# Performance work log

Hardware: AMD Instinct MI355X
Metric: run time of the kernel (lower is better)

The kernel has to match this reference:

```python
import jax, jax.numpy as jnp
import numpy as np

B, S, I, H = 64, 512, 512, 512


def setup_inputs() -> dict:
    key = jax.random.key(0)
    ks = jax.random.split(key, 5)
    scale = 1.0 / np.sqrt(I + H)  # keep gates out of hard saturation
    return {
        "x": jax.random.normal(ks[0], (B, S, I), dtype=jnp.float32),
        "h": jax.random.normal(ks[1], (B, H), dtype=jnp.float32),
        "W_r": jax.random.normal(ks[2], (H, I + H), dtype=jnp.float32) * scale,
        "b_r": jnp.zeros((H,), dtype=jnp.float32),
        "W_z": jax.random.normal(ks[3], (H, I + H), dtype=jnp.float32) * scale,
        "b_z": jnp.zeros((H,), dtype=jnp.float32),
        "W_h": jax.random.normal(ks[4], (H, I + H), dtype=jnp.float32) * scale,
        "b_h": jnp.zeros((H,), dtype=jnp.float32),
    }


def reference(x, h, W_r, b_r, W_z, b_z, W_h, b_h):
    # Split each [H, I+H] weight into input part and hidden part (torch cat order: [x, h]).
    i = x.shape[-1]
    Wr_x, Wr_h = W_r[:, :i], W_r[:, i:]
    Wz_x, Wz_h = W_z[:, :i], W_z[:, i:]
    Wh_x, Wh_h = W_h[:, :i], W_h[:, i:]

    # Precompute the input contributions for all timesteps in one big GEMM each.
    xr = jnp.einsum("bsi,hi->bsh", x, Wr_x) + b_r  # [B,S,H]
    xz = jnp.einsum("bsi,hi->bsh", x, Wz_x) + b_z
    xh = jnp.einsum("bsi,hi->bsh", x, Wh_x) + b_h

    def step(h, inp):
        xr_t, xz_t, xh_t = inp  # each [B,H]
        r = jax.nn.sigmoid(xr_t + h @ Wr_h.T)
        z = jax.nn.sigmoid(xz_t + h @ Wz_h.T)
        h_tilde = jnp.tanh(xh_t + (r * h) @ Wh_h.T)
        h_new = (1.0 - z) * h + z * h_tilde
        return h_new, h_new

    # time-major for scan
    xs = (xr.transpose(1, 0, 2), xz.transpose(1, 0, 2), xh.transpose(1, 0, 2))
    h_last, ys = jax.lax.scan(step, h, xs)
    y = ys.transpose(1, 0, 2)  # [B,S,H]; dropout p=0 -> identity
    return y, h_last
```

## Files before the change

### kernel.cpp

```cpp
#include <hip/hip_runtime.h>

#define B_ 64
#define S_ 512
#define H_ 512

typedef unsigned short u16;
typedef unsigned int   u32;
typedef unsigned long long u64;

typedef __attribute__((ext_vector_type(8))) short    bf16x8;
typedef __attribute__((ext_vector_type(8))) _Float16 f16x8;
typedef __attribute__((ext_vector_type(4))) float    f32x4;
typedef __attribute__((ext_vector_type(2))) _Float16 h2_t;

#define PJ_GATE ((size_t)512 * 64 * 512)

__device__ inline u16 f2bf(float f) {
  u32 u = __builtin_bit_cast(u32, f);
  u32 r = (u + 0x7fffu + ((u >> 16) & 1u)) >> 16;
  return (u16)r;
}
__device__ inline u32 pkbf2(float a, float b) {
  return (u32)f2bf(a) | ((u32)f2bf(b) << 16);
}
__device__ inline u16 f2h(float a) {
  _Float16 x = (_Float16)a;
  return __builtin_bit_cast(u16, x);
}
__device__ inline u32 pk2h(float a, float b) {
  return (u32)f2h(a) | ((u32)f2h(b) << 16);
}
__device__ inline float sigmoidf_(float x) { return 1.f / (1.f + __expf(-x)); }
__device__ inline float tanhf_(float x) {
  float e = __expf(-2.f * fabsf(x));
  float t = (1.f - e) / (1.f + e);
  return copysignf(t, x);
}
__device__ inline void xstore64(u64* p, u64 v) {
  __hip_atomic_store(p, v, __ATOMIC_RELAXED, __HIP_MEMORY_SCOPE_AGENT);
}
__device__ inline u64 xload(const u64* p) {
  return __hip_atomic_load(p, __ATOMIC_RELAXED, __HIP_MEMORY_SCOPE_AGENT);
}

__global__ void k_convert_w(const float* __restrict__ Wr, const float* __restrict__ Wz,
                            const float* __restrict__ Wh, uint4* __restrict__ WF) {
  int g = blockIdx.y;
  const float* Ws = (g == 0) ? Wr : ((g == 1) ? Wz : Wh);
  int i = blockIdx.x * 256 + threadIdx.x;
  int lane = i & 63;
  int kt   = (i >> 6) & 15;
  int rt   = i >> 10;
  int row  = rt * 16 + (lane & 15);
  int col  = 512 + kt * 32 + (lane >> 4) * 8;
  const float* src = Ws + (size_t)row * 1024 + col;
  float4 a = *(const float4*)src;
  float4 b = *(const float4*)(src + 4);
  uint4 o;
  o.x = pk2h(a.x, a.y); o.y = pk2h(a.z, a.w);
  o.z = pk2h(b.x, b.y); o.w = pk2h(b.z, b.w);
  WF[((size_t)(g * 32 + rt) * 16 + kt) * 64 + lane] = o;
}

__global__ __launch_bounds__(256) void k_proj_gemm(
    const float* __restrict__ x,
    const float* __restrict__ Wr, const float* __restrict__ Wz, const float* __restrict__ Wh,
    const float* __restrict__ br, const float* __restrict__ bz, const float* __restrict__ bh,
    u16* __restrict__ P)
{
  const int g  = blockIdx.z;
  const int bm = blockIdx.x * 64;
  const int bn = blockIdx.y * 64;
  const float* Ws = (g == 0) ? Wr : ((g == 1) ? Wz : Wh);
  __shared__ __align__(16) u16 As[64][32];
  __shared__ __align__(16) u16 Bs[64][32];
  const int tid  = threadIdx.x;
  const int lane = tid & 63;
  const int wm   = (tid >> 6) >> 1;
  const int wn   = (tid >> 6) & 1;
  const int srow = tid >> 2;
  const int scol = (tid & 3) * 8;

  f32x4 zero4 = {0.f, 0.f, 0.f, 0.f};
  f32x4 acc[2][2];
  acc[0][0] = zero4; acc[0][1] = zero4; acc[1][0] = zero4; acc[1][1] = zero4;

  for (int k0 = 0; k0 < 512; k0 += 32) {
    __syncthreads();
    {
      const float* xs = x + (size_t)(bm + srow) * 512 + k0 + scol;
      float4 a = *(const float4*)xs, b = *(const float4*)(xs + 4);
      uint4 av; av.x = pkbf2(a.x, a.y); av.y = pkbf2(a.z, a.w);
      av.z = pkbf2(b.x, b.y); av.w = pkbf2(b.z, b.w);
      *(uint4*)(&As[srow][scol]) = av;
      const float* wsrc = Ws + (size_t)(bn + srow) * 1024 + k0 + scol;
      float4 c = *(const float4*)wsrc, d = *(const float4*)(wsrc + 4);
      uint4 bv; bv.x = pkbf2(c.x, c.y); bv.y = pkbf2(c.z, c.w);
      bv.z = pkbf2(d.x, d.y); bv.w = pkbf2(d.z, d.w);
      *(uint4*)(&Bs[srow][scol]) = bv;
    }
    __syncthreads();
#pragma unroll
    for (int mi = 0; mi < 2; ++mi) {
      bf16x8 a = *(const bf16x8*)(&As[wm * 32 + mi * 16 + (lane & 15)][(lane >> 4) * 8]);
#pragma unroll
      for (int ni = 0; ni < 2; ++ni) {
        bf16x8 b = *(const bf16x8*)(&Bs[wn * 32 + ni * 16 + (lane & 15)][(lane >> 4) * 8]);
        acc[mi][ni] = __builtin_amdgcn_mfma_f32_16x16x32_bf16(a, b, acc[mi][ni], 0, 0, 0);
      }
    }
  }
  const float* bias = (g == 0) ? br : ((g == 1) ? bz : bh);
#pragma unroll
  for (int mi = 0; mi < 2; ++mi)
#pragma unroll
    for (int ni = 0; ni < 2; ++ni) {
      int col  = bn + wn * 32 + ni * 16 + (lane & 15);
      float bv = bias[col];
#pragma unroll
      for (int r = 0; r < 4; ++r) {
        int row = bm + wm * 32 + mi * 16 + (lane >> 4) * 4 + r;
        int bb = row >> 9, ss = row & 511;
        float v = acc[mi][ni][r] + bv;
        P[((size_t)g * 512 + ss) * (64 * 512) + (size_t)bb * 512 + col] =
            __builtin_bit_cast(u16, (_Float16)v);
      }
    }
}

__global__ __launch_bounds__(512, 2) void k_gru_scan(
    const float* __restrict__ h0,
    const u16*  __restrict__ P,
    const uint4* __restrict__ WF,
    u32* __restrict__ RHX,
    u32* __restrict__ HX,
    float* __restrict__ y,
    float* __restrict__ hlast)
{
  const int q = blockIdx.x & 3;
  const int c = blockIdx.x >> 2;
  const int t = threadIdx.x;
  const int w = t >> 6;
  const int l = t & 63;
  const int bq = l & 15;
  const int g4 = l >> 4;
  const int bglob = c * 16 + bq;
  const int rt  = q * 8 + w;
  const int j0A = q * 128 + w * 16 + g4 * 4;

  __shared__ __align__(16) u16 whlds[8 * 16 * 512];
  __shared__ __align__(16) u16 hbuf[16 * 520];

  f16x8 wr[16], wz[16];
#pragma unroll
  for (int kt = 0; kt < 16; ++kt) {
    wr[kt] = __builtin_bit_cast(f16x8, WF[((size_t)(0 * 32 + rt) * 16 + kt) * 64 + l]);
    wz[kt] = __builtin_bit_cast(f16x8, WF[((size_t)(1 * 32 + rt) * 16 + kt) * 64 + l]);
    *(uint4*)&whlds[((w * 16 + kt) * 64 + l) * 8] =
        WF[((size_t)(2 * 32 + rt) * 16 + kt) * 64 + l];
  }
#pragma unroll
  for (int kt = 0; kt < 16; ++kt)
    asm volatile("" : "+v"(wr[kt]), "+v"(wz[kt]));

  f32x4 hold = *(const f32x4*)(h0 + (size_t)bglob * 512 + j0A);
  {
    int b = t >> 5, j = (t & 31) * 16;
    const float4* s = (const float4*)(h0 + (size_t)(c * 16 + b) * 512 + j);
    float4 v0 = s[0], v1 = s[1], v2 = s[2], v3 = s[3];
    uint4 o0, o1;
    o0.x = pk2h(v0.x, v0.y); o0.y = pk2h(v0.z, v0.w);
    o0.z = pk2h(v1.x, v1.y); o0.w = pk2h(v1.z, v1.w);
    o1.x = pk2h(v2.x, v2.y); o1.y = pk2h(v2.z, v2.w);
    o1.z = pk2h(v3.x, v3.y); o1.w = pk2h(v3.z, v3.w);
    uint4* d = (uint4*)&hbuf[b * 520 + j];
    d[0] = o0; d[1] = o1;
  }
  __syncthreads();

  const u16* Ppr = P + (size_t)bglob * 512 + j0A;
  const u16* Ppz = P + PJ_GATE + (size_t)bglob * 512 + j0A;
  const u16* Pph = P + 2 * PJ_GATE + (size_t)bglob * 512 + j0A;

  const int bR = t >> 5;
  const int kR = (t & 31) * 4;
  const int k1 = ((q + 1) & 3) * 128 + kR;
  const int k2 = ((q + 2) & 3) * 128 + kR;
  const int k3 = ((q + 3) & 3) * 128 + kR;
  const int CL  = 16 * 512;
  const int PAR = 4 * CL;

  uint2 pru = *(const uint2*)Ppr;
  uint2 pzu = *(const uint2*)Ppz;

#define POLL_INTO_HBUF(Xp)                                                      \
  {                                                                             \
    const u64* p1 = (const u64*)((Xp) + bR * 512 + k1);                         \
    const u64* p2 = (const u64*)((Xp) + bR * 512 + k2);                         \
    const u64* p3 = (const u64*)((Xp) + bR * 512 + k3);                         \
    u64 A1 = xload(p1), B1 = xload(p1 + 1);                                     \
    u64 A2 = xload(p2), B2 = xload(p2 + 1);                                     \
    u64 A3 = xload(p3), B3 = xload(p3 + 1);                                     \
    while (((A1 ^ tp) & TMASK) != 0ull) { __builtin_amdgcn_s_sleep(1); A1 = xload(p1); } \
    while (((B1 ^ tp) & TMASK) != 0ull) { __builtin_amdgcn_s_sleep(1); B1 = xload(p1 + 1); } \
    while (((A2 ^ tp) & TMASK) != 0ull) { __builtin_amdgcn_s_sleep(1); A2 = xload(p2); } \
    while (((B2 ^ tp) & TMASK) != 0ull) { __builtin_amdgcn_s_sleep(1); B2 = xload(p2 + 1); } \
    while (((A3 ^ tp) & TMASK) != 0ull) { __builtin_amdgcn_s_sleep(1); A3 = xload(p3); } \
    while (((B3 ^ tp) & TMASK) != 0ull) { __builtin_amdgcn_s_sleep(1); B3 = xload(p3 + 1); } \
    uint2 w1, w2, w3;                                                           \
    w1.x = (u32)(A1 & 0xffffu) | (((u32)(A1 >> 32) & 0xffffu) << 16);           \
    w1.y = (u32)(B1 & 0xffffu) | (((u32)(B1 >> 32) & 0xffffu) << 16);           \
    w2.x = (u32)(A2 & 0xffffu) | (((u32)(A2 >> 32) & 0xffffu) << 16);           \
    w2.y = (u32)(B2 & 0xffffu) | (((u32)(B2 >> 32) & 0xffffu) << 16);           \
    w3.x = (u32)(A3 & 0xffffu) | (((u32)(A3 >> 32) & 0xffffu) << 16);           \
    w3.y = (u32)(B3 & 0xffffu) | (((u32)(B3 >> 32) & 0xffffu) << 16);           \
    *(uint2*)&hbuf[bR * 520 + k1] = w1;                                         \
    *(uint2*)&hbuf[bR * 520 + k2] = w2;                                         \
    *(uint2*)&hbuf[bR * 520 + k3] = w3;                                         \
  }

  const u64 TMASK = 0xffff0000ffff0000ull;

  for (int ts = 0; ts < S_; ++ts) {
    const int par = ts & 1;
    const u32 tag = (u32)(ts + 1);
    const u64 tp  = ((u64)tag << 16) | ((u64)tag << 48);
    u32* RHXp = RHX + par * PAR + c * CL;
    u32* HXp  = HX  + par * PAR + c * CL;

    uint2 phu = *(const uint2*)(Pph + (size_t)ts * 32768);

    f32x4 ar = {0.f, 0.f, 0.f, 0.f}, az = {0.f, 0.f, 0.f, 0.f};
#pragma unroll
    for (int kt = 0; kt < 16; ++kt) {
      f16x8 hv = *(const f16x8*)&hbuf[bq * 520 + g4 * 8 + kt * 32];
      ar = __builtin_amdgcn_mfma_f32_16x16x32_f16(wr[kt], hv, ar, 0, 0, 0);
      az = __builtin_amdgcn_mfma_f32_16x16x32_f16(wz[kt], hv, az, 0, 0, 0);
    }
    h2_t pr0 = __builtin_bit_cast(h2_t, pru.x), pr1 = __builtin_bit_cast(h2_t, pru.y);
    h2_t pz0 = __builtin_bit_cast(h2_t, pzu.x), pz1 = __builtin_bit_cast(h2_t, pzu.y);
    float rr0 = sigmoidf_(ar[0] + (float)pr0[0]);
    float rr1 = sigmoidf_(ar[1] + (float)pr0[1]);
    float rr2 = sigmoidf_(ar[2] + (float)pr1[0]);
    float rr3 = sigmoidf_(ar[3] + (float)pr1[1]);
    float zz0 = sigmoidf_(az[0] + (float)pz0[0]);
    float zz1 = sigmoidf_(az[1] + (float)pz0[1]);
    float zz2 = sigmoidf_(az[2] + (float)pz1[0]);
    float zz3 = sigmoidf_(az[3] + (float)pz1[1]);
    u16 rh0 = f2h(rr0 * hold[0]), rh1 = f2h(rr1 * hold[1]);
    u16 rh2 = f2h(rr2 * hold[2]), rh3 = f2h(rr3 * hold[3]);
    {
      u64 v01 = (u64)((tag << 16) | rh0) | ((u64)((tag << 16) | rh1) << 32);
      u64 v23 = (u64)((tag << 16) | rh2) | ((u64)((tag << 16) | rh3) << 32);
      xstore64((u64*)(RHXp + bq * 512 + j0A), v01);
      xstore64((u64*)(RHXp + bq * 512 + j0A + 2), v23);
    }
    __syncthreads();
    *(uint2*)&hbuf[bq * 520 + j0A] =
        uint2{(u32)rh0 | ((u32)rh1 << 16), (u32)rh2 | ((u32)rh3 << 16)};
    POLL_INTO_HBUF(RHXp)
    __syncthreads();

    f32x4 ah = {0.f, 0.f, 0.f, 0.f};
#pragma unroll
    for (int kt = 0; kt < 16; ++kt) {
      f16x8 rv = *(const f16x8*)&hbuf[bq * 520 + g4 * 8 + kt * 32];
      f16x8 wh = *(const f16x8*)&whlds[((w * 16 + kt) * 64 + l) * 8];
      ah = __builtin_amdgcn_mfma_f32_16x16x32_f16(wh, rv, ah, 0, 0, 0);
    }
    h2_t ph0 = __builtin_bit_cast(h2_t, phu.x), ph1 = __builtin_bit_cast(h2_t, phu.y);
    float ht0 = tanhf_(ah[0] + (float)ph0[0]);
    float ht1 = tanhf_(ah[1] + (float)ph0[1]);
    float ht2 = tanhf_(ah[2] + (float)ph1[0]);
    float ht3 = tanhf_(ah[3] + (float)ph1[1]);
    f32x4 hn;
    hn[0] = zz0 * ht0 + (1.f - zz0) * hold[0];
    hn[1] = zz1 * ht1 + (1.f - zz1) * hold[1];
    hn[2] = zz2 * ht2 + (1.f - zz2) * hold[2];
    hn[3] = zz3 * ht3 + (1.f - zz3) * hold[3];
    hold = hn;
    __builtin_nontemporal_store(hn,
        (f32x4*)(y + (size_t)bglob * 262144 + (size_t)ts * 512 + j0A));
    u16 h0b = f2h(hn[0]), h1b = f2h(hn[1]), h2b = f2h(hn[2]), h3b = f2h(hn[3]);
    {
      u64 v01 = (u64)((tag << 16) | h0b) | ((u64)((tag << 16) | h1b) << 32);
      u64 v23 = (u64)((tag << 16) | h2b) | ((u64)((tag << 16) | h3b) << 32);
      xstore64((u64*)(HXp + bq * 512 + j0A), v01);
      xstore64((u64*)(HXp + bq * 512 + j0A + 2), v23);
    }

    {
      int tsn = (ts < S_ - 1) ? ts + 1 : ts;
      pru = *(const uint2*)(Ppr + (size_t)tsn * 32768);
      pzu = *(const uint2*)(Ppz + (size_t)tsn * 32768);
    }

    __syncthreads();
    *(uint2*)&hbuf[bq * 520 + j0A] =
        uint2{(u32)h0b | ((u32)h1b << 16), (u32)h2b | ((u32)h3b << 16)};
    POLL_INTO_HBUF(HXp)
    __syncthreads();
  }

  *(f32x4*)(hlast + (size_t)bglob * 512 + j0A) = hold;
}

extern "C" void kernel_launch(void* const* d_in, const int* in_sizes, int n_in,
                              void* d_out, int out_size, void* d_ws, size_t ws_size,
                              hipStream_t stream) {
  const float* x  = (const float*)d_in[0];
  const float* h0 = (const float*)d_in[1];
  const float* Wr = (const float*)d_in[2];
  const float* br = (const float*)d_in[3];
  const float* Wz = (const float*)d_in[4];
  const float* bz = (const float*)d_in[5];
  const float* Wh = (const float*)d_in[6];
  const float* bh = (const float*)d_in[7];

  char* ws = (char*)d_ws;
  uint4* WF  = (uint4*)ws;
  u16*   P   = (u16*)(ws + 2097152);
  u32*   RHX = (u32*)(ws + 102760448);
  u32*   HX  = (u32*)(ws + 103022592);

  float* y     = (float*)d_out;
  float* hlast = y + (size_t)B_ * S_ * H_;

  hipMemsetAsync(ws + 102760448, 0, 524288, stream);
  k_convert_w<<<dim3(128, 3), dim3(256), 0, stream>>>(Wr, Wz, Wh, WF);
  k_proj_gemm<<<dim3(512, 8, 3), dim3(256), 0, stream>>>(x, Wr, Wz, Wh, br, bz, bh, P);
  k_gru_scan<<<dim3(16), dim3(512), 0, stream>>>(h0, P, WF, RHX, HX, y, hlast);
}
```

Before: 3.552 ms.

## Split GRU scan across 32 blocks with per-wave gate specialization

The recurrent scan kernel now runs 32 blocks instead of 16, 8 per batch chunk. Each block owns 64 hidden columns instead of 128, and its wave groups are split so half compute the r gate and half the z gate. The W_h hidden matmul is split along K between the two wave groups and reduced through LDS, and its weights move from LDS into registers. Polling now has each thread load 8 contiguous tagged words for the full row. This halves per-block MFMA work on the serial critical path, at the cost of more cross-block synchronization traffic, more blocks polling, and an extra LDS reduction and barrier each step.

```diff
diff --git a/kernel.cpp b/kernel.cpp
--- a/kernel.cpp
+++ b/kernel.cpp
@@ -14,6 +14,7 @@
 typedef __attribute__((ext_vector_type(2))) _Float16 h2_t;
 
 #define PJ_GATE ((size_t)512 * 64 * 512)
+#define TMASK 0xffff0000ffff0000ull
 
 __device__ inline u16 f2bf(float f) {
   u32 u = __builtin_bit_cast(u32, f);
@@ -41,6 +42,29 @@
 }
 __device__ inline u64 xload(const u64* p) {
   return __hip_atomic_load(p, __ATOMIC_RELAXED, __HIP_MEMORY_SCOPE_AGENT);
+}
+__device__ inline void pub4(u32* gp, u32 taghi, f32x4 v) {
+  u64 a = (u64)(taghi | f2h(v[0])) | ((u64)(taghi | f2h(v[1])) << 32);
+  u64 b = (u64)(taghi | f2h(v[2])) | ((u64)(taghi | f2h(v[3])) << 32);
+  xstore64((u64*)gp, a);
+  xstore64((u64*)(gp + 2), b);
+}
+__device__ inline void poll8_to_lds(const u32* gbase, u16* lbase, u64 tp) {
+  const u64* p = (const u64*)gbase;
+  u64 v[8];
+#pragma unroll
+  for (int i = 0; i < 8; ++i) v[i] = xload(p + i);
+#pragma unroll
+  for (int i = 0; i < 8; ++i)
+    while ((v[i] ^ tp) & TMASK) { __builtin_amdgcn_s_sleep(1); v[i] = xload(p + i); }
+  u32 pk[8];
+#pragma unroll
+  for (int i = 0; i < 8; ++i)
+    pk[i] = (u32)(v[i] & 0xffffu) | (((u32)(v[i] >> 32)) << 16);
+  uint4 a = {pk[0], pk[1], pk[2], pk[3]};
+  uint4 b = {pk[4], pk[5], pk[6], pk[7]};
+  *(uint4*)(lbase) = a;
+  *(uint4*)(lbase + 8) = b;
 }
 
 __global__ void k_convert_w(const float* __restrict__ Wr, const float* __restrict__ Wz,
@@ -128,7 +152,9 @@
     }
 }
 
-__global__ __launch_bounds__(512, 2) void k_gru_scan(
+__global__ __attribute__((amdgpu_flat_work_group_size(512, 512),
+                          amdgpu_waves_per_eu(2, 2)))
+void k_gru_scan(
     const float* __restrict__ h0,
     const u16*  __restrict__ P,
     const uint4* __restrict__ WF,
@@ -137,33 +163,41 @@
     float* __restrict__ y,
     float* __restrict__ hlast)
 {
-  const int q = blockIdx.x & 3;
-  const int c = blockIdx.x >> 2;
+  const int q = blockIdx.x & 7;
+  const int c = blockIdx.x >> 3;
   const int t = threadIdx.x;
   const int w = t >> 6;
   const int l = t & 63;
   const int bq = l & 15;
   const int g4 = l >> 4;
-  const int bglob = c * 16 + bq;
-  const int rt  = q * 8 + w;
-  const int j0A = q * 128 + w * 16 + g4 * 4;
-
-  __shared__ __align__(16) u16 whlds[8 * 16 * 512];
+  const int g1 = w >> 2;
+  const int wl = w & 3;
+  const int rtile = q * 4 + wl;
+  const int jrow = q * 64 + wl * 16 + g4 * 4;
+  const int jloc = wl * 16 + g4 * 4;
+  const int bgA = c * 16 + bq;
+
   __shared__ __align__(16) u16 hbuf[16 * 520];
-
-  f16x8 wr[16], wz[16];
-#pragma unroll
-  for (int kt = 0; kt < 16; ++kt) {
-    wr[kt] = __builtin_bit_cast(f16x8, WF[((size_t)(0 * 32 + rt) * 16 + kt) * 64 + l]);
-    wz[kt] = __builtin_bit_cast(f16x8, WF[((size_t)(1 * 32 + rt) * 16 + kt) * 64 + l]);
-    *(uint4*)&whlds[((w * 16 + kt) * 64 + l) * 8] =
-        WF[((size_t)(2 * 32 + rt) * 16 + kt) * 64 + l];
-  }
+  __shared__ __align__(16) u16 rhbuf[16 * 520];
+  __shared__ float zbuf[64][16];
+  __shared__ __align__(16) f32x4 pLDS[4][64];
+
+  f16x8 wa[16], whf[8];
 #pragma unroll
   for (int kt = 0; kt < 16; ++kt)
-    asm volatile("" : "+v"(wr[kt]), "+v"(wz[kt]));
-
-  f32x4 hold = *(const f32x4*)(h0 + (size_t)bglob * 512 + j0A);
+    wa[kt] = __builtin_bit_cast(f16x8, WF[((size_t)(g1 * 32 + rtile) * 16 + kt) * 64 + l]);
+#pragma unroll
+  for (int i = 0; i < 8; ++i)
+    whf[i] = __builtin_bit_cast(f16x8,
+        WF[((size_t)(2 * 32 + rtile) * 16 + (g1 * 8 + i)) * 64 + l]);
+#pragma unroll
+  for (int kt = 0; kt < 16; ++kt)
+    asm volatile("" : "+v"(wa[kt]));
+#pragma unroll
+  for (int i = 0; i < 8; ++i)
+    asm volatile("" : "+v"(whf[i]));
+
+  f32x4 hreg = *(const f32x4*)(h0 + (size_t)bgA * 512 + jrow);
   {
     int b = t >> 5, j = (t & 31) * 16;
     const float4* s = (const float4*)(h0 + (size_t)(c * 16 + b) * 512 + j);
@@ -178,131 +212,90 @@
   }
   __syncthreads();
 
-  const u16* Ppr = P + (size_t)bglob * 512 + j0A;
-  const u16* Ppz = P + PJ_GATE + (size_t)bglob * 512 + j0A;
-  const u16* Pph = P + 2 * PJ_GATE + (size_t)bglob * 512 + j0A;
+  const u16* Pg  = P + (size_t)g1 * PJ_GATE + (size_t)bgA * 512 + jrow;
+  const u16* Pph = P + 2 * PJ_GATE + (size_t)bgA * 512 + jrow;
 
   const int bR = t >> 5;
-  const int kR = (t & 31) * 4;
-  const int k1 = ((q + 1) & 3) * 128 + kR;
-  const int k2 = ((q + 2) & 3) * 128 + kR;
-  const int k3 = ((q + 3) & 3) * 128 + kR;
+  const int jR = (t & 31) * 16;
   const int CL  = 16 * 512;
   const int PAR = 4 * CL;
 
-  uint2 pru = *(const uint2*)Ppr;
-  uint2 pzu = *(const uint2*)Ppz;
-
-#define POLL_INTO_HBUF(Xp)                                                      \
-  {                                                                             \
-    const u64* p1 = (const u64*)((Xp) + bR * 512 + k1);                         \
-    const u64* p2 = (const u64*)((Xp) + bR * 512 + k2);                         \
-    const u64* p3 = (const u64*)((Xp) + bR * 512 + k3);                         \
-    u64 A1 = xload(p1), B1 = xload(p1 + 1);                                     \
-    u64 A2 = xload(p2), B2 = xload(p2 + 1);                                     \
-    u64 A3 = xload(p3), B3 = xload(p3 + 1);                                     \
-    while (((A1 ^ tp) & TMASK) != 0ull) { __builtin_amdgcn_s_sleep(1); A1 = xload(p1); } \
-    while (((B1 ^ tp) & TMASK) != 0ull) { __builtin_amdgcn_s_sleep(1); B1 = xload(p1 + 1); } \
-    while (((A2 ^ tp) & TMASK) != 0ull) { __builtin_amdgcn_s_sleep(1); A2 = xload(p2); } \
-    while (((B2 ^ tp) & TMASK) != 0ull) { __builtin_amdgcn_s_sleep(1); B2 = xload(p2 + 1); } \
-    while (((A3 ^ tp) & TMASK) != 0ull) { __builtin_amdgcn_s_sleep(1); A3 = xload(p3); } \
-    while (((B3 ^ tp) & TMASK) != 0ull) { __builtin_amdgcn_s_sleep(1); B3 = xload(p3 + 1); } \
-    uint2 w1, w2, w3;                                                           \
-    w1.x = (u32)(A1 & 0xffffu) | (((u32)(A1 >> 32) & 0xffffu) << 16);           \
-    w1.y = (u32)(B1 & 0xffffu) | (((u32)(B1 >> 32) & 0xffffu) << 16);           \
-    w2.x = (u32)(A2 & 0xffffu) | (((u32)(A2 >> 32) & 0xffffu) << 16);           \
-    w2.y = (u32)(B2 & 0xffffu) | (((u32)(B2 >> 32) & 0xffffu) << 16);           \
-    w3.x = (u32)(A3 & 0xffffu) | (((u32)(A3 >> 32) & 0xffffu) << 16);           \
-    w3.y = (u32)(B3 & 0xffffu) | (((u32)(B3 >> 32) & 0xffffu) << 16);           \
-    *(uint2*)&hbuf[bR * 520 + k1] = w1;                                         \
-    *(uint2*)&hbuf[bR * 520 + k2] = w2;                                         \
-    *(uint2*)&hbuf[bR * 520 + k3] = w3;                                         \
-  }
-
-  const u64 TMASK = 0xffff0000ffff0000ull;
+  uint2 pgu = *(const uint2*)Pg;
 
   for (int ts = 0; ts < S_; ++ts) {
     const int par = ts & 1;
-    const u32 tag = (u32)(ts + 1);
-    const u64 tp  = ((u64)tag << 16) | ((u64)tag << 48);
+    const u32 taghi = (u32)(ts + 1) << 16;
+    const u64 tp = (u64)taghi | ((u64)taghi << 32);
     u32* RHXp = RHX + par * PAR + c * CL;
     u32* HXp  = HX  + par * PAR + c * CL;
 
-    uint2 phu = *(const uint2*)(Pph + (size_t)ts * 32768);
-
-    f32x4 ar = {0.f, 0.f, 0.f, 0.f}, az = {0.f, 0.f, 0.f, 0.f};
+    uint2 phu = {0, 0};
+    if (g1 == 0) phu = *(const uint2*)(Pph + (size_t)ts * 32768);
+
+    f32x4 aa = {0.f, 0.f, 0.f, 0.f};
 #pragma unroll
     for (int kt = 0; kt < 16; ++kt) {
       f16x8 hv = *(const f16x8*)&hbuf[bq * 520 + g4 * 8 + kt * 32];
-      ar = __builtin_amdgcn_mfma_f32_16x16x32_f16(wr[kt], hv, ar, 0, 0, 0);
-      az = __builtin_amdgcn_mfma_f32_16x16x32_f16(wz[kt], hv, az, 0, 0, 0);
-    }
-    h2_t pr0 = __builtin_bit_cast(h2_t, pru.x), pr1 = __builtin_bit_cast(h2_t, pru.y);
-    h2_t pz0 = __builtin_bit_cast(h2_t, pzu.x), pz1 = __builtin_bit_cast(h2_t, pzu.y);
-    float rr0 = sigmoidf_(ar[0] + (float)pr0[0]);
-    float rr1 = sigmoidf_(ar[1] + (float)pr0[1]);
-    float rr2 = sigmoidf_(ar[2] + (float)pr1[0]);
-    float rr3 = sigmoidf_(ar[3] + (float)pr1[1]);
-    float zz0 = sigmoidf_(az[0] + (float)pz0[0]);
-    float zz1 = sigmoidf_(az[1] + (float)pz0[1]);
-    float zz2 = sigmoidf_(az[2] + (float)pz1[0]);
-    float zz3 = sigmoidf_(az[3] + (float)pz1[1]);
-    u16 rh0 = f2h(rr0 * hold[0]), rh1 = f2h(rr1 * hold[1]);
-    u16 rh2 = f2h(rr2 * hold[2]), rh3 = f2h(rr3 * hold[3]);
-    {
-      u64 v01 = (u64)((tag << 16) | rh0) | ((u64)((tag << 16) | rh1) << 32);
-      u64 v23 = (u64)((tag << 16) | rh2) | ((u64)((tag << 16) | rh3) << 32);
-      xstore64((u64*)(RHXp + bq * 512 + j0A), v01);
-      xstore64((u64*)(RHXp + bq * 512 + j0A + 2), v23);
-    }
-    __syncthreads();
-    *(uint2*)&hbuf[bq * 520 + j0A] =
-        uint2{(u32)rh0 | ((u32)rh1 << 16), (u32)rh2 | ((u32)rh3 << 16)};
-    POLL_INTO_HBUF(RHXp)
-    __syncthreads();
-
-    f32x4 ah = {0.f, 0.f, 0.f, 0.f};
-#pragma unroll
-    for (int kt = 0; kt < 16; ++kt) {
-      f16x8 rv = *(const f16x8*)&hbuf[bq * 520 + g4 * 8 + kt * 32];
-      f16x8 wh = *(const f16x8*)&whlds[((w * 16 + kt) * 64 + l) * 8];
-      ah = __builtin_amdgcn_mfma_f32_16x16x32_f16(wh, rv, ah, 0, 0, 0);
-    }
-    h2_t ph0 = __builtin_bit_cast(h2_t, phu.x), ph1 = __builtin_bit_cast(h2_t, phu.y);
-    float ht0 = tanhf_(ah[0] + (float)ph0[0]);
-    float ht1 = tanhf_(ah[1] + (float)ph0[1]);
-    float ht2 = tanhf_(ah[2] + (float)ph1[0]);
-    float ht3 = tanhf_(ah[3] + (float)ph1[1]);
-    f32x4 hn;
-    hn[0] = zz0 * ht0 + (1.f - zz0) * hold[0];
-    hn[1] = zz1 * ht1 + (1.f - zz1) * hold[1];
-    hn[2] = zz2 * ht2 + (1.f - zz2) * hold[2];
-    hn[3] = zz3 * ht3 + (1.f - zz3) * hold[3];
-    hold = hn;
-    __builtin_nontemporal_store(hn,
-        (f32x4*)(y + (size_t)bglob * 262144 + (size_t)ts * 512 + j0A));
-    u16 h0b = f2h(hn[0]), h1b = f2h(hn[1]), h2b = f2h(hn[2]), h3b = f2h(hn[3]);
-    {
-      u64 v01 = (u64)((tag << 16) | h0b) | ((u64)((tag << 16) | h1b) << 32);
-      u64 v23 = (u64)((tag << 16) | h2b) | ((u64)((tag << 16) | h3b) << 32);
-      xstore64((u64*)(HXp + bq * 512 + j0A), v01);
-      xstore64((u64*)(HXp + bq * 512 + j0A + 2), v23);
-    }
-
+      aa = __builtin_amdgcn_mfma_f32_16x16x32_f16(wa[kt], hv, aa, 0, 0, 0);
+    }
+    h2_t pg0 = __builtin_bit_cast(h2_t, pgu.x), pg1 = __builtin_bit_cast(h2_t, pgu.y);
+    float v0 = sigmoidf_(aa[0] + (float)pg0[0]);
+    float v1 = sigmoidf_(aa[1] + (float)pg0[1]);
+    float v2 = sigmoidf_(aa[2] + (float)pg1[0]);
+    float v3 = sigmoidf_(aa[3] + (float)pg1[1]);
+    if (g1 == 0) {
+      f32x4 rh = {v0 * hreg[0], v1 * hreg[1], v2 * hreg[2], v3 * hreg[3]};
+      pub4(RHXp + bq * 512 + jrow, taghi, rh);
+    } else {
+      zbuf[jloc + 0][bq] = v0;
+      zbuf[jloc + 1][bq] = v1;
+      zbuf[jloc + 2][bq] = v2;
+      zbuf[jloc + 3][bq] = v3;
+    }
     {
       int tsn = (ts < S_ - 1) ? ts + 1 : ts;
-      pru = *(const uint2*)(Ppr + (size_t)tsn * 32768);
-      pzu = *(const uint2*)(Ppz + (size_t)tsn * 32768);
-    }
-
-    __syncthreads();
-    *(uint2*)&hbuf[bq * 520 + j0A] =
-        uint2{(u32)h0b | ((u32)h1b << 16), (u32)h2b | ((u32)h3b << 16)};
-    POLL_INTO_HBUF(HXp)
+      pgu = *(const uint2*)(Pg + (size_t)tsn * 32768);
+    }
+
+    poll8_to_lds(RHXp + bR * 512 + jR, &rhbuf[bR * 520 + jR], tp);
+    __syncthreads();
+
+    f32x4 pb = {0.f, 0.f, 0.f, 0.f};
+#pragma unroll
+    for (int i = 0; i < 8; ++i) {
+      int kt = g1 * 8 + i;
+      f16x8 rv = *(const f16x8*)&rhbuf[bq * 520 + g4 * 8 + kt * 32];
+      pb = __builtin_amdgcn_mfma_f32_16x16x32_f16(whf[i], rv, pb, 0, 0, 0);
+    }
+    if (g1 == 1) pLDS[wl][l] = pb;
+    __syncthreads();
+
+    if (g1 == 0) {
+      f32x4 s = pb + pLDS[wl][l];
+      h2_t ph0 = __builtin_bit_cast(h2_t, phu.x), ph1 = __builtin_bit_cast(h2_t, phu.y);
+      float ht0 = tanhf_(s[0] + (float)ph0[0]);
+      float ht1 = tanhf_(s[1] + (float)ph0[1]);
+      float ht2 = tanhf_(s[2] + (float)ph1[0]);
+      float ht3 = tanhf_(s[3] + (float)ph1[1]);
+      float z0 = zbuf[jloc + 0][bq], z1 = zbuf[jloc + 1][bq];
+      float z2 = zbuf[jloc + 2][bq], z3 = zbuf[jloc + 3][bq];
+      f32x4 hn;
+      hn[0] = z0 * ht0 + (1.f - z0) * hreg[0];
+      hn[1] = z1 * ht1 + (1.f - z1) * hreg[1];
+      hn[2] = z2 * ht2 + (1.f - z2) * hreg[2];
+      hn[3] = z3 * ht3 + (1.f - z3) * hreg[3];
+      hreg = hn;
+      pub4(HXp + bq * 512 + jrow, taghi, hn);
+      __builtin_nontemporal_store(hn,
+          (f32x4*)(y + ((size_t)bgA * 512 + ts) * 512 + jrow));
+    }
+
+    poll8_to_lds(HXp + bR * 512 + jR, &hbuf[bR * 520 + jR], tp);
     __syncthreads();
   }
 
-  *(f32x4*)(hlast + (size_t)bglob * 512 + j0A) = hold;
+  if (g1 == 0)
+    *(f32x4*)(hlast + (size_t)bgA * 512 + jrow) = hreg;
 }
 
 extern "C" void kernel_launch(void* const* d_in, const int* in_sizes, int n_in,
@@ -326,8 +319,8 @@
   float* y     = (float*)d_out;
   float* hlast = y + (size_t)B_ * S_ * H_;
 
-  hipMemsetAsync(ws + 102760448, 0, 524288, stream);
+  (void)hipMemsetAsync(ws + 102760448, 0, 524288, stream);
   k_convert_w<<<dim3(128, 3), dim3(256), 0, stream>>>(Wr, Wz, Wh, WF);
   k_proj_gemm<<<dim3(512, 8, 3), dim3(256), 0, stream>>>(x, Wr, Wz, Wh, br, bz, bh, P);
-  k_gru_scan<<<dim3(16), dim3(512), 0, stream>>>(h0, P, WF, RHX, HX, y, hlast);
-}
+  k_gru_scan<<<dim3(32), dim3(512), 0, stream>>>(h0, P, WF, RHX, HX, y, hlast);
+}
```

After: 5.272 ms. 48.4% more time.

## Keep Wh in registers, swizzle hbuf into MFMA fragment order, defer z-gate

Applied to the files above, without the earlier changes.

The candidate-gate weights move from LDS into VGPRs alongside Wr and Wz, which removes the per-step LDS weight reads in the third matmul. The hidden-state buffer is re-laid out in MFMA fragment order so each lane reads a contiguous 16-byte chunk per k-tile. The z-gate matmul is moved after the r*h stores, so it overlaps with the latency of the cross-block exchange. The y store is placed after the exchange stores. Holding 48 fragment registers per lane raises VGPR pressure and risks spilling.

```diff
diff --git a/kernel.cpp b/kernel.cpp
--- a/kernel.cpp
+++ b/kernel.cpp
@@ -41,6 +41,9 @@
 }
 __device__ inline u64 xload(const u64* p) {
   return __hip_atomic_load(p, __ATOMIC_RELAXED, __HIP_MEMORY_SCOPE_AGENT);
+}
+__device__ inline int fragAddr(int j, int b) {
+  return ((j >> 5) << 9) + ((b + (((j & 31) >> 3) << 4)) << 3) + (j & 7);
 }
 
 __global__ void k_convert_w(const float* __restrict__ Wr, const float* __restrict__ Wz,
@@ -147,21 +150,17 @@
   const int bglob = c * 16 + bq;
   const int rt  = q * 8 + w;
   const int j0A = q * 128 + w * 16 + g4 * 4;
-
-  __shared__ __align__(16) u16 whlds[8 * 16 * 512];
-  __shared__ __align__(16) u16 hbuf[16 * 520];
-
-  f16x8 wr[16], wz[16];
+  const int ownA = fragAddr(j0A, bq);
+
+  __shared__ __align__(16) u16 hbuf[16 * 512];
+
+  f16x8 wr[16], wz[16], wh[16];
 #pragma unroll
   for (int kt = 0; kt < 16; ++kt) {
     wr[kt] = __builtin_bit_cast(f16x8, WF[((size_t)(0 * 32 + rt) * 16 + kt) * 64 + l]);
     wz[kt] = __builtin_bit_cast(f16x8, WF[((size_t)(1 * 32 + rt) * 16 + kt) * 64 + l]);
-    *(uint4*)&whlds[((w * 16 + kt) * 64 + l) * 8] =
-        WF[((size_t)(2 * 32 + rt) * 16 + kt) * 64 + l];
-  }
-#pragma unroll
-  for (int kt = 0; kt < 16; ++kt)
-    asm volatile("" : "+v"(wr[kt]), "+v"(wz[kt]));
+    wh[kt] = __builtin_bit_cast(f16x8, WF[((size_t)(2 * 32 + rt) * 16 + kt) * 64 + l]);
+  }
 
   f32x4 hold = *(const f32x4*)(h0 + (size_t)bglob * 512 + j0A);
   {
@@ -173,8 +172,8 @@
     o0.z = pk2h(v1.x, v1.y); o0.w = pk2h(v1.z, v1.w);
     o1.x = pk2h(v2.x, v2.y); o1.y = pk2h(v2.z, v2.w);
     o1.z = pk2h(v3.x, v3.y); o1.w = pk2h(v3.z, v3.w);
-    uint4* d = (uint4*)&hbuf[b * 520 + j];
-    d[0] = o0; d[1] = o1;
+    *(uint4*)&hbuf[fragAddr(j, b)]     = o0;
+    *(uint4*)&hbuf[fragAddr(j + 8, b)] = o1;
   }
   __syncthreads();
 
@@ -187,6 +186,9 @@
   const int k1 = ((q + 1) & 3) * 128 + kR;
   const int k2 = ((q + 2) & 3) * 128 + kR;
   const int k3 = ((q + 3) & 3) * 128 + kR;
+  const int a1 = fragAddr(k1, bR);
+  const int a2 = fragAddr(k2, bR);
+  const int a3 = fragAddr(k3, bR);
   const int CL  = 16 * 512;
   const int PAR = 4 * CL;
 
@@ -214,9 +216,9 @@
     w2.y = (u32)(B2 & 0xffffu) | (((u32)(B2 >> 32) & 0xffffu) << 16);           \
     w3.x = (u32)(A3 & 0xffffu) | (((u32)(A3 >> 32) & 0xffffu) << 16);           \
     w3.y = (u32)(B3 & 0xffffu) | (((u32)(B3 >> 32) & 0xffffu) << 16);           \
-    *(uint2*)&hbuf[bR * 520 + k1] = w1;                                         \
-    *(uint2*)&hbuf[bR * 520 + k2] = w2;                                         \
-    *(uint2*)&hbuf[bR * 520 + k3] = w3;                                         \
+    *(uint2*)&hbuf[a1] = w1;                                                    \
+    *(uint2*)&hbuf[a2] = w2;                                                    \
+    *(uint2*)&hbuf[a3] = w3;                                                    \
   }
 
   const u64 TMASK = 0xffff0000ffff0000ull;
@@ -230,23 +232,17 @@
 
     uint2 phu = *(const uint2*)(Pph + (size_t)ts * 32768);
 
-    f32x4 ar = {0.f, 0.f, 0.f, 0.f}, az = {0.f, 0.f, 0.f, 0.f};
+    f32x4 ar = {0.f, 0.f, 0.f, 0.f};
 #pragma unroll
     for (int kt = 0; kt < 16; ++kt) {
-      f16x8 hv = *(const f16x8*)&hbuf[bq * 520 + g4 * 8 + kt * 32];
+      f16x8 hv = *(const f16x8*)&hbuf[(kt << 9) + (l << 3)];
       ar = __builtin_amdgcn_mfma_f32_16x16x32_f16(wr[kt], hv, ar, 0, 0, 0);
-      az = __builtin_amdgcn_mfma_f32_16x16x32_f16(wz[kt], hv, az, 0, 0, 0);
     }
     h2_t pr0 = __builtin_bit_cast(h2_t, pru.x), pr1 = __builtin_bit_cast(h2_t, pru.y);
-    h2_t pz0 = __builtin_bit_cast(h2_t, pzu.x), pz1 = __builtin_bit_cast(h2_t, pzu.y);
     float rr0 = sigmoidf_(ar[0] + (float)pr0[0]);
     float rr1 = sigmoidf_(ar[1] + (float)pr0[1]);
     float rr2 = sigmoidf_(ar[2] + (float)pr1[0]);
     float rr3 = sigmoidf_(ar[3] + (float)pr1[1]);
-    float zz0 = sigmoidf_(az[0] + (float)pz0[0]);
-    float zz1 = sigmoidf_(az[1] + (float)pz0[1]);
-    float zz2 = sigmoidf_(az[2] + (float)pz1[0]);
-    float zz3 = sigmoidf_(az[3] + (float)pz1[1]);
     u16 rh0 = f2h(rr0 * hold[0]), rh1 = f2h(rr1 * hold[1]);
     u16 rh2 = f2h(rr2 * hold[2]), rh3 = f2h(rr3 * hold[3]);
     {
@@ -255,8 +251,21 @@
       xstore64((u64*)(RHXp + bq * 512 + j0A), v01);
       xstore64((u64*)(RHXp + bq * 512 + j0A + 2), v23);
     }
-    __syncthreads();
-    *(uint2*)&hbuf[bq * 520 + j0A] =
+
+    f32x4 az = {0.f, 0.f, 0.f, 0.f};
+#pragma unroll
+    for (int kt = 0; kt < 16; ++kt) {
+      f16x8 hv = *(const f16x8*)&hbuf[(kt << 9) + (l << 3)];
+      az = __builtin_amdgcn_mfma_f32_16x16x32_f16(wz[kt], hv, az, 0, 0, 0);
+    }
+    h2_t pz0 = __builtin_bit_cast(h2_t, pzu.x), pz1 = __builtin_bit_cast(h2_t, pzu.y);
+    float zz0 = sigmoidf_(az[0] + (float)pz0[0]);
+    float zz1 = sigmoidf_(az[1] + (float)pz0[1]);
+    float zz2 = sigmoidf_(az[2] + (float)pz1[0]);
+    float zz3 = sigmoidf_(az[3] + (float)pz1[1]);
+
+    __syncthreads();
+    *(uint2*)&hbuf[ownA] =
         uint2{(u32)rh0 | ((u32)rh1 << 16), (u32)rh2 | ((u32)rh3 << 16)};
     POLL_INTO_HBUF(RHXp)
     __syncthreads();
@@ -264,9 +273,8 @@
     f32x4 ah = {0.f, 0.f, 0.f, 0.f};
 #pragma unroll
     for (int kt = 0; kt < 16; ++kt) {
-      f16x8 rv = *(const f16x8*)&hbuf[bq * 520 + g4 * 8 + kt * 32];
-      f16x8 wh = *(const f16x8*)&whlds[((w * 16 + kt) * 64 + l) * 8];
-      ah = __builtin_amdgcn_mfma_f32_16x16x32_f16(wh, rv, ah, 0, 0, 0);
+      f16x8 rv = *(const f16x8*)&hbuf[(kt << 9) + (l << 3)];
+      ah = __builtin_amdgcn_mfma_f32_16x16x32_f16(wh[kt], rv, ah, 0, 0, 0);
     }
     h2_t ph0 = __builtin_bit_cast(h2_t, phu.x), ph1 = __builtin_bit_cast(h2_t, phu.y);
     float ht0 = tanhf_(ah[0] + (float)ph0[0]);
@@ -279,8 +287,6 @@
     hn[2] = zz2 * ht2 + (1.f - zz2) * hold[2];
     hn[3] = zz3 * ht3 + (1.f - zz3) * hold[3];
     hold = hn;
-    __builtin_nontemporal_store(hn,
-        (f32x4*)(y + (size_t)bglob * 262144 + (size_t)ts * 512 + j0A));
     u16 h0b = f2h(hn[0]), h1b = f2h(hn[1]), h2b = f2h(hn[2]), h3b = f2h(hn[3]);
     {
       u64 v01 = (u64)((tag << 16) | h0b) | ((u64)((tag << 16) | h1b) << 32);
@@ -288,6 +294,8 @@
       xstore64((u64*)(HXp + bq * 512 + j0A), v01);
       xstore64((u64*)(HXp + bq * 512 + j0A + 2), v23);
     }
+    __builtin_nontemporal_store(hn,
+        (f32x4*)(y + (size_t)bglob * 262144 + (size_t)ts * 512 + j0A));
 
     {
       int tsn = (ts < S_ - 1) ? ts + 1 : ts;
@@ -296,7 +304,7 @@
     }
 
     __syncthreads();
-    *(uint2*)&hbuf[bq * 520 + j0A] =
+    *(uint2*)&hbuf[ownA] =
         uint2{(u32)h0b | ((u32)h1b << 16), (u32)h2b | ((u32)h3b << 16)};
     POLL_INTO_HBUF(HXp)
     __syncthreads();
@@ -326,7 +334,7 @@
   float* y     = (float*)d_out;
   float* hlast = y + (size_t)B_ * S_ * H_;
 
-  hipMemsetAsync(ws + 102760448, 0, 524288, stream);
+  (void)hipMemsetAsync(ws + 102760448, 0, 524288, stream);
   k_convert_w<<<dim3(128, 3), dim3(256), 0, stream>>>(Wr, Wz, Wh, WF);
   k_proj_gemm<<<dim3(512, 8, 3), dim3(256), 0, stream>>>(x, Wr, Wz, Wh, br, bz, bh, P);
   k_gru_scan<<<dim3(16), dim3(512), 0, stream>>>(h0, P, WF, RHX, HX, y, hlast);
```

New measurement: 4.622 ms. 1.3x slower.
